# Performance work log

Hardware: AMD Instinct MI355X
Metric: run time of the kernel (lower is better)

Reference implementation:

```python
import jax, jax.numpy as jnp
import numpy as np


def _pairwise_sq(x, y):
    # squared euclidean distances [B,N,M] via gram trick (avoids [B,N,M,D] temp)
    x2 = jnp.sum(x * x, -1)[:, :, None]
    y2 = jnp.sum(y * y, -1)[:, None, :]
    return x2 + y2 - 2.0 * jnp.einsum('bnd,bmd->bnm', x, y)


def _dtw_dp(C):
    # Subsequence DTW accumulated-cost matrix. C: [N,M].
    # D[0,:] = C[0,:] (free start anywhere in y);
    # D[i,j] = C[i,j] + min(D[i-1,j], D[i-1,j-1], D[i,j-1]).
    # Within-row recurrence D[i,j] = min(a[j], D[i,j-1] + C[i,j]) with
    # a[j] = min(D[i-1,j], D[i-1,j-1]) + C[i,j] is a min-plus prefix scan:
    # D[i,j] = S[j] + cummin(a - S)[j], S = cumsum(C[i]).
    inf = jnp.asarray(jnp.inf, C.dtype)
    def row(Dprev, Crow):
        shifted = jnp.concatenate([jnp.full((1,), inf, C.dtype), Dprev[:-1]])
        a = jnp.minimum(Dprev, shifted) + Crow
        S = jnp.cumsum(Crow)
        D = S + jax.lax.cummin(a - S)
        return D, D
    _, Dr = jax.lax.scan(row, C[0], C[1:])
    return jnp.concatenate([C[0][None], Dr], 0)


def _backtrack(D):
    # Backtrack optimal subseq-DTW path from (N-1, argmin D[-1]) to row 0.
    # Returns, per x index i, the largest y index aligned to i on the path
    # (== last occurrence kept by dict(dtw_path) in the torch code).
    N, M = D.shape
    inf = jnp.asarray(jnp.inf, D.dtype)
    j0 = jnp.argmin(D[-1]).astype(jnp.int32)
    i0 = jnp.asarray(N - 1, jnp.int32)
    yl = jnp.zeros((N,), jnp.int32).at[i0].set(j0)
    def step(carry, _):
        i, j, yl = carry
        dd = jnp.where(j > 0, D[i - 1, j - 1], inf)
        du = D[i - 1, j]
        dl = jnp.where(j > 0, D[i, j - 1], inf)
        best = jnp.minimum(jnp.minimum(dd, du), dl)
        take_d = dd == best
        take_u = (~take_d) & (du == best)
        ni = jnp.where(take_d | take_u, i - 1, i)
        nj = jnp.where(take_d, j - 1, jnp.where(take_u, j, j - 1))
        active = i > 0
        ni = jnp.where(active, ni, i)
        nj = jnp.where(active, nj, j)
        yl = jnp.where(active, yl.at[ni].max(nj), yl)
        return (ni, nj, yl), None
    (_, _, yl), _ = jax.lax.scan(step, (i0, j0, yl), None, length=N + M)
    return yl


def setup_inputs() -> dict:
    key = jax.random.key(0)
    k0, k1, k2, k3 = jax.random.split(key, 4)
    B, N, M, D = 16, 1024, 4096, 64
    return {
        'x': jax.random.normal(k0, (B, N, D), jnp.float32),
        'y': jax.random.normal(k1, (B, M, D), jnp.float32),
        'x_t': jax.random.uniform(k2, (B, N), dtype=jnp.float32),
        'y_t': jax.random.uniform(k3, (B, M), dtype=jnp.float32),
    }


def reference(x, y, x_t, y_t):
    C = _pairwise_sq(x, y)                      # [B,N,M]
    D = jax.vmap(_dtw_dp)(C)                    # [B,N,M]
    # total path cost == DP optimum (sum of C along the optimal path)
    dtw_cost = jnp.min(D[:, -1, :], axis=-1)    # [B]
    y_last = jax.vmap(_backtrack)(jax.lax.stop_gradient(D))  # [B,N] int32
    w_ts = x_t                                  # path covers all x indices 0..N-1 in order
    w_vs = jnp.take_along_axis(y_t, y_last, axis=1)
    return dtw_cost, w_ts, w_vs
```

## Files before the change

### kernel.cpp

```cpp
#include <hip/hip_runtime.h>

#define B_ 16
#define N_ 1024
#define M_ 4096
#define D_ 64
#define SROWS_ (N_ + 63)
#define SROWSP_ (SROWS_ + 17)
#define SPAIR_ 544
#define TSB_ ((size_t)SPAIR_ * 128)
#define BTQ_ 96
#define BTROWS_ 128

__device__ __forceinline__ float finf() { return __builtin_inff(); }

__device__ __forceinline__ float wave_shr1(float x) {
  return __int_as_float(__builtin_amdgcn_update_dpp(
      0, __float_as_int(x), 0x138, 0xF, 0xF, false));
}
__device__ __forceinline__ float rdlane(float v, int l) {
  return __int_as_float(__builtin_amdgcn_readlane(__float_as_int(v), l));
}

__global__ void prep_kernel(const float* __restrict__ x,
                            const float* __restrict__ x_t,
                            float* __restrict__ x2,
                            float* __restrict__ w_ts_out) {
  int id = blockIdx.x * blockDim.x + threadIdx.x;
  const float4* xr = (const float4*)(x + (size_t)id * D_);
  float s = 0.f;
#pragma unroll
  for (int e = 0; e < D_ / 4; ++e) {
    float4 v = xr[e];
    s += v.x * v.x + v.y * v.y + v.z * v.z + v.w * v.w;
  }
  x2[id] = s;
  w_ts_out[id] = x_t[id];
}

__global__ __launch_bounds__(256) void gemm_kernel(
    const float* __restrict__ x, const float* __restrict__ y,
    const float* __restrict__ x2, float* __restrict__ Cs, int chunkBase) {
  const int b = blockIdx.z;
  const int tile = blockIdx.x;
  const int t = threadIdx.x;
  const int cg = t & 63;
  const int rg = t >> 6;
  const int ibeg = blockIdx.y * 32;
  float* CsT = Cs + (size_t)(b * 4 + tile) * SROWSP_ * 256;

  __shared__ float4 ylds[16 * 256];
  __shared__ float4 xlds[16 * 32];
  __shared__ float y2lds[256];

  {
    const int j = chunkBase + tile * 256 + t;
    const float4* yrow = (const float4*)(y + ((size_t)b * M_ + j) * D_);
    float4 yr[16];
#pragma unroll
    for (int e = 0; e < 16; ++e) yr[e] = yrow[e];
    float y2 = 0.f;
#pragma unroll
    for (int e = 0; e < 16; ++e)
      y2 += yr[e].x * yr[e].x + yr[e].y * yr[e].y + yr[e].z * yr[e].z +
            yr[e].w * yr[e].w;
    y2lds[t] = y2;
#pragma unroll
    for (int e = 0; e < 16; ++e) ylds[e * 256 + t] = yr[e];
  }
  if (t < 128) {
    const int row = t >> 2;
    const int part = t & 3;
    const float4* xr = (const float4*)(x + ((size_t)b * N_ + ibeg + row) * D_);
#pragma unroll
    for (int k = 0; k < 4; ++k) {
      const int e = part * 4 + k;
      xlds[e * 32 + row] = xr[e];
    }
  }
  __syncthreads();

  const int r0 = rg * 8;
  float acc[8][4];
#pragma unroll
  for (int r = 0; r < 8; ++r)
#pragma unroll
    for (int c = 0; c < 4; ++c) acc[r][c] = 0.f;

#pragma unroll
  for (int kb = 0; kb < 4; ++kb) {
    float4 yf[4][4];
#pragma unroll
    for (int c = 0; c < 4; ++c)
#pragma unroll
      for (int ee = 0; ee < 4; ++ee)
        yf[c][ee] = ylds[(kb * 4 + ee) * 256 + cg + 64 * c];
#pragma unroll
    for (int r = 0; r < 8; ++r) {
      float4 xv[4];
#pragma unroll
      for (int ee = 0; ee < 4; ++ee)
        xv[ee] = xlds[(kb * 4 + ee) * 32 + r0 + r];
#pragma unroll
      for (int ee = 0; ee < 4; ++ee) {
#pragma unroll
        for (int c = 0; c < 4; ++c) {
          acc[r][c] += xv[ee].x * yf[c][ee].x + xv[ee].y * yf[c][ee].y +
                       xv[ee].z * yf[c][ee].z + xv[ee].w * yf[c][ee].w;
        }
      }
    }
  }

#pragma unroll
  for (int r = 0; r < 8; ++r) {
    const int i = ibeg + r0 + r;
    const float xx = x2[b * N_ + i];
#pragma unroll
    for (int c = 0; c < 4; ++c) {
      const int ct = cg + 64 * c;
      const int l = ct >> 2;
      CsT[(size_t)(i + l) * 256 + ct] = xx + y2lds[ct] - 2.f * acc[r][c];
    }
  }
}

__global__ __launch_bounds__(256) void dtw_dp(
    const float* __restrict__ Cs, unsigned char* __restrict__ dec,
    const float* __restrict__ carryIn, float* __restrict__ carryOut,
    float* __restrict__ partV, int* __restrict__ partJ,
    int chunk, int hasCarry) {
  const int b = blockIdx.x;
  const int t = threadIdx.x;
  const int lane = t & 63;
  const int W = t >> 6;

  __shared__ float ring[3][1024];
  __shared__ float cring[1024];
  __shared__ int prog[3];
  __shared__ float redV[4];
  __shared__ int redJ[4];
  volatile int* vProg = prog;

  if (t < 3) prog[t] = -1;
  const float* cIn = carryIn + b * N_;
  if (hasCarry) ((float4*)cring)[t] = ((const float4*)cIn)[t];
  __syncthreads();

  const float INF = finf();
  const float* loadP = Cs + (size_t)(b * 4 + W) * SROWSP_ * 256;
  const int tileG = chunk * 4 + W;
  unsigned short* decP =
      (unsigned short*)(dec + (size_t)(b * 16 + tileG) * TSB_) + lane;
  float* carryB = carryOut + b * N_;
  const int jbase = tileG * 256 + lane * 4;

  float4 cc0 = ((const float4*)(loadP + 0 * 256))[lane];
  float4 cc1 = ((const float4*)(loadP + 1 * 256))[lane];
  float4 cc2 = ((const float4*)(loadP + 2 * 256))[lane];
  float4 cc3 = ((const float4*)(loadP + 3 * 256))[lane];
  float4 cc4 = ((const float4*)(loadP + 4 * 256))[lane];
  float4 cc5 = ((const float4*)(loadP + 5 * 256))[lane];
  float4 cc6 = ((const float4*)(loadP + 6 * 256))[lane];
  float4 cc7 = ((const float4*)(loadP + 7 * 256))[lane];
  loadP += 8 * 256;

  float edgeVec = INF, lvPrev = INF;
  float up0 = 0.f, up1 = 0.f, up2 = 0.f, up3 = 0.f;
  float dpp1 = INF, dpp2 = INF;
  float fin0 = INF, fin1 = INF, fin2 = INF, fin3 = INF;
  float ebuf[8];

#define SUPERHEAD()                                                           \
  {                                                                           \
    if (W > 0) {                                                              \
      if (sb < N_) {                                                          \
        const int tgt = sb + 63;                                              \
        while (vProg[W - 1] < tgt) {}                                         \
        asm volatile("" ::: "memory");                                        \
        edgeVec = ring[W - 1][(sb + lane) & 1023];                            \
      }                                                                       \
    } else if (hasCarry) {                                                    \
      if (sb < N_) edgeVec = cring[(sb + lane) & 1023];                       \
    }                                                                         \
  }

#define DPSTEP(KK, CCV, ROW0, FIN)                                            \
  {                                                                           \
    const float lv = rdlane(edgeVec, u0 + (KK));                              \
    const float left = (lane == 0) ? lv : dpp1;                               \
    const float diag = (lane == 0) ? lvPrev : dpp2;                           \
    lvPrev = lv;                                                              \
    float bv0 = fminf(diag, fminf(up0, left));                                \
    unsigned int pk = (diag <= bv0) ? 0u : ((up0 <= bv0) ? 1u : 2u);          \
    if (ROW0) bv0 = (sb + (KK) == lane) ? 0.f : bv0;                          \
    const float D0 = CCV.x + bv0;                                             \
    float bv1 = fminf(up0, fminf(up1, D0));                                   \
    pk |= (up0 <= bv1) ? 0u : ((up1 <= bv1) ? 4u : 8u);                       \
    if (ROW0) bv1 = (sb + (KK) == lane) ? 0.f : bv1;                          \
    const float D1 = CCV.y + bv1;                                             \
    float bv2 = fminf(up1, fminf(up2, D1));                                   \
    pk |= (up1 <= bv2) ? 0u : ((up2 <= bv2) ? 16u : 32u);                     \
    if (ROW0) bv2 = (sb + (KK) == lane) ? 0.f : bv2;                          \
    const float D2 = CCV.z + bv2;                                             \
    float bv3 = fminf(up2, fminf(up3, D2));                                   \
    pk |= (up2 <= bv3) ? 0u : ((up3 <= bv3) ? 64u : 128u);                    \
    if (ROW0) bv3 = (sb + (KK) == lane) ? 0.f : bv3;                          \
    const float D3 = CCV.w + bv3;                                             \
    ebuf[(KK)] = D3;                                                          \
    if ((KK) & 1) {                                                           \
      pk16 |= pk << 8;                                                        \
      decP[((KK) >> 1) * 64] = (unsigned short)pk16;                          \
    } else {                                                                  \
      pk16 = pk;                                                              \
    }                                                                         \
    if (FIN) {                                                                \
      const bool lr = (sb + (KK) == 1023 + lane);                             \
      fin0 = lr ? D0 : fin0; fin1 = lr ? D1 : fin1;                           \
      fin2 = lr ? D2 : fin2; fin3 = lr ? D3 : fin3;                           \
    }                                                                         \
    const float sh = wave_shr1(D3);                                           \
    dpp2 = dpp1; dpp1 = sh;                                                   \
    up0 = D0; up1 = D1; up2 = D2; up3 = D3;                                   \
    CCV = ((const float4*)(loadP + (KK) * 256))[lane];                        \
  }

#define BLOCKEND()                                                            \
  {                                                                           \
    const int r0 = sb - 63;                                                   \
    if (W < 3) {                                                              \
      if (lane == 63 && r0 > -8 && r0 < N_) {                                 \
        _Pragma("unroll") for (int k = 0; k < 8; ++k) {                       \
          const int r = r0 + k;                                               \
          if ((unsigned)r < (unsigned)N_) ring[W][r] = ebuf[k];               \
        }                                                                     \
        __builtin_amdgcn_s_waitcnt(0xC07F);                                   \
        vProg[W] = r0 + 7;                                                    \
      }                                                                       \
    } else if (chunk < 3) {                                                   \
      if (lane == 63 && r0 > -8 && r0 < N_) {                                 \
        _Pragma("unroll") for (int k = 0; k < 8; ++k) {                       \
          const int r = r0 + k;                                               \
          if ((unsigned)r < (unsigned)N_) carryB[r] = ebuf[k];                \
        }                                                                     \
      }                                                                       \
    }                                                                         \
    loadP += 8 * 256;                                                         \
    decP += 256;                                                              \
  }

#define STEP8(R0, FN)                                                         \
  DPSTEP(0, cc0, R0, FN) DPSTEP(1, cc1, R0, FN) DPSTEP(2, cc2, R0, FN)        \
  DPSTEP(3, cc3, R0, FN) DPSTEP(4, cc4, R0, FN) DPSTEP(5, cc5, R0, FN)        \
  DPSTEP(6, cc6, R0, FN) DPSTEP(7, cc7, R0, FN)

  int sb = 0;
  {
    SUPERHEAD();
    for (int blk = 0; blk < 8; ++blk) {
      const int u0 = blk * 8;
      unsigned int pk16;
      STEP8(1, 0)
      BLOCKEND();
      sb += 8;
    }
  }
  for (int sup = 1; sup < 15; ++sup) {
    SUPERHEAD();
    for (int blk = 0; blk < 8; ++blk) {
      const int u0 = blk * 8;
      unsigned int pk16;
      STEP8(0, 0)
      BLOCKEND();
      sb += 8;
    }
  }
  for (int sup = 15; sup < 17; ++sup) {
    SUPERHEAD();
    for (int blk = 0; blk < 8; ++blk) {
      const int u0 = blk * 8;
      unsigned int pk16;
      STEP8(0, 1)
      BLOCKEND();
      sb += 8;
    }
  }
#undef DPSTEP
#undef STEP8
#undef SUPERHEAD
#undef BLOCKEND

  float mv = fin0; int mj = jbase;
  if (fin1 < mv) { mv = fin1; mj = jbase + 1; }
  if (fin2 < mv) { mv = fin2; mj = jbase + 2; }
  if (fin3 < mv) { mv = fin3; mj = jbase + 3; }
#pragma unroll
  for (int off = 32; off > 0; off >>= 1) {
    const float ov = __shfl_down(mv, off);
    const int oj = __shfl_down(mj, off);
    if (ov < mv || (ov == mv && oj < mj)) { mv = ov; mj = oj; }
  }
  if (lane == 0) { redV[W] = mv; redJ[W] = mj; }
  __syncthreads();
  if (t == 0) {
    float bm = redV[0]; int bj = redJ[0];
#pragma unroll
    for (int w = 1; w < 4; ++w)
      if (redV[w] < bm) { bm = redV[w]; bj = redJ[w]; }
    partV[b * 4 + chunk] = bm;
    partJ[b * 4 + chunk] = bj;
  }
}

__global__ __launch_bounds__(64) void backtrack_kernel(
    const unsigned char* __restrict__ dec, const float* __restrict__ partV,
    const int* __restrict__ partJ, int nch, const float* __restrict__ y_t,
    float* __restrict__ w_vs, float* __restrict__ cost_out) {
  const int b = blockIdx.x;
  const int lane = threadIdx.x;
  __shared__ unsigned int stage[3 * 3072];
  __shared__ unsigned short tab[BTROWS_][BTQ_ * 4 + 2];
  __shared__ int st_i, st_j;
  __shared__ int jrow[BTROWS_ + 1];
  const unsigned char* db = dec + (size_t)b * 16 * TSB_;
  const float* yt = y_t + b * M_;
  float* wv = w_vs + b * N_;

  if (lane == 0) {
    float bc = finf(); int bj = 0;
    for (int c = 0; c < nch; ++c) {
      const float v = partV[b * nch + c];
      const int j = partJ[b * nch + c];
      if (v < bc) { bc = v; bj = j; }
    }
    cost_out[b] = bc;
    st_i = N_ - 1;
    st_j = bj;
    wv[N_ - 1] = yt[bj];
  }
  for (;;) {
    __syncthreads();
    const int i = st_i, j = st_j;
    if (i <= 0) break;
    const int qj = j >> 2;
    int qlo = qj - (BTQ_ - 1);
    if (qlo < 0) qlo = 0;
    const int Tbase = qlo >> 6;
    int plo = (i - 127) >> 1;
    if (plo < 0) plo = 0;

#pragma unroll
    for (int tt = 0; tt < 3; ++tt) {
      int T = Tbase + tt;
      if (T > 15) T = 15;
      const uint4* src =
          (const uint4*)(db + (size_t)T * TSB_ + (size_t)plo * 128);
#pragma unroll
      for (int v = 0; v < 12; ++v) {
        const int wb = tt * 12288 + (v * 64 + lane) * 16;
        const int sw = wb ^ (((wb >> 7) & 7) << 4);
        *(uint4*)((char*)stage + sw) = src[v * 64 + lane];
      }
    }
    __syncthreads();

    const unsigned char* sb8 = (const unsigned char*)stage;
#pragma unroll
    for (int half = 0; half < 2; ++half) {
      const int r = i - lane - half * 64;
      if (r >= 1) {
        unsigned char wr[BTQ_];
#pragma unroll
        for (int k = 0; k < BTQ_; ++k) {
          const int q = qlo + k;
          const int tt = (q >> 6) - Tbase;
          const int l = q & 63;
          const int s = r + l;
          int idx = tt * 12288 + ((s >> 1) - plo) * 128 + l * 2 + (s & 1);
          idx ^= ((idx >> 7) & 7) << 4;
          wr[k] = sb8[idx];
        }
        unsigned short run = 0xFFFF;
        const int tr = lane + half * 64;
#pragma unroll
        for (int k = 0; k < BTQ_; ++k) {
          const unsigned int byte = wr[k];
#pragma unroll
          for (int cs = 0; cs < 4; ++cs) {
            const unsigned int code = (byte >> (2 * cs)) & 3u;
            const int c = 4 * k + cs;
            const unsigned short v =
                (code != 2u) ? (unsigned short)((c << 2) | code) : run;
            tab[tr][c] = v;
            run = v;
          }
        }
      }
    }
    __syncthreads();
    if (lane == 0) {
      const int base = qlo << 2;
      int rr = i, cj = j;
      while (rr >= 1 && (i - rr) < BTROWS_) {
        const int l = i - rr;
        const int c = cj - base;
        if (c < 0) break;
        const unsigned short v = tab[l][c];
        if (v == 0xFFFF) { cj = base - 1; break; }
        const int e = v >> 2;
        const int ce = v & 3;
        cj = base + e - (ce == 0 ? 1 : 0);
        --rr;
        jrow[i - rr] = cj;
      }
      st_i = rr;
      st_j = cj;
    }
    __syncthreads();
    const int cnt = i - st_i;
    if (lane < cnt) wv[i - 1 - lane] = yt[jrow[lane + 1]];
    {
      const int l2 = lane + 64;
      if (l2 < cnt) wv[i - 1 - l2] = yt[jrow[l2 + 1]];
    }
  }
}

extern "C" void kernel_launch(void* const* d_in, const int* in_sizes, int n_in,
                              void* d_out, int out_size, void* d_ws, size_t ws_size,
                              hipStream_t stream) {
  const float* x = (const float*)d_in[0];
  const float* y = (const float*)d_in[1];
  const float* x_t = (const float*)d_in[2];
  const float* y_t = (const float*)d_in[3];

  float* out_cost = (float*)d_out;
  float* out_wts = out_cost + B_;
  float* out_wvs = out_wts + B_ * N_;

  const size_t csBytes = (size_t)B_ * 4 * SROWSP_ * 256 * 4;
  const size_t decBytes = (size_t)B_ * 16 * TSB_;
  const size_t x2Bytes = (size_t)B_ * N_ * 4;

  char* ws = (char*)d_ws;
  float* Cs = (float*)ws;
  unsigned char* dec = (unsigned char*)(ws + csBytes);
  float* x2 = (float*)(ws + csBytes + decBytes);
  float* carryA = (float*)(ws + csBytes + decBytes + x2Bytes);
  float* carryB = carryA + B_ * N_;
  float* partV = carryB + B_ * N_;
  int* partJ = (int*)(partV + B_ * 4);

  prep_kernel<<<dim3((B_ * N_) / 256), 256, 0, stream>>>(x, x_t, x2, out_wts);

  float* cbuf[2] = {carryA, carryB};
  for (int c = 0; c < 4; ++c) {
    gemm_kernel<<<dim3(4, N_ / 32, B_), 256, 0, stream>>>(x, y, x2, Cs,
                                                          c * 1024);
    const float* cin = cbuf[(c + 1) & 1];
    float* cout = cbuf[c & 1];
    dtw_dp<<<dim3(B_), 256, 0, stream>>>(Cs, dec, cin, cout, partV, partJ, c,
                                         c > 0 ? 1 : 0);
  }

  backtrack_kernel<<<dim3(B_), 64, 0, stream>>>(dec, partV, partJ, 4, y_t,
                                                out_wvs, out_cost);
}
```

Baseline: 1.258 ms.

## Pack two batches per DTW block and sync wave pipeline per 8-row block

The DTW wavefront kernel now runs two batch elements per 512-thread workgroup, halving the grid to 8 blocks, with per-group LDS rings and progress flags. Inter-wave synchronization now waits for only 8 new rows of the previous wave's edge values before each 8-row block, instead of 64 rows per super-block. This shortens pipeline fill latency between the four wavefronts. It also co-locates two batches on one CU. That may increase contention or reduce parallelism across CUs, and it adds more frequent spin-waits and edge reloads.

```diff
diff --git a/kernel.cpp b/kernel.cpp
--- a/kernel.cpp
+++ b/kernel.cpp
@@ -4,6 +4,7 @@
 #define N_ 1024
 #define M_ 4096
 #define D_ 64
+#define NB_ 2
 #define SROWS_ (N_ + 63)
 #define SROWSP_ (SROWS_ + 17)
 #define SPAIR_ 544
@@ -124,26 +125,28 @@
   }
 }
 
-__global__ __launch_bounds__(256) void dtw_dp(
+__global__ __launch_bounds__(512) void dtw_dp(
     const float* __restrict__ Cs, unsigned char* __restrict__ dec,
     const float* __restrict__ carryIn, float* __restrict__ carryOut,
     float* __restrict__ partV, int* __restrict__ partJ,
     int chunk, int hasCarry) {
-  const int b = blockIdx.x;
   const int t = threadIdx.x;
-  const int lane = t & 63;
-  const int W = t >> 6;
-
-  __shared__ float ring[3][1024];
-  __shared__ float cring[1024];
-  __shared__ int prog[3];
-  __shared__ float redV[4];
-  __shared__ int redJ[4];
-  volatile int* vProg = prog;
-
-  if (t < 3) prog[t] = -1;
+  const int tb = t & 255;
+  const int G = t >> 8;
+  const int b = blockIdx.x * NB_ + G;
+  const int lane = tb & 63;
+  const int W = tb >> 6;
+
+  __shared__ float ring[NB_][3][1024];
+  __shared__ float cring[NB_][1024];
+  __shared__ int prog[NB_][3];
+  __shared__ float redV[NB_][4];
+  __shared__ int redJ[NB_][4];
+  volatile int* vProg = prog[G];
+
+  if (tb < 3) prog[G][tb] = -1;
   const float* cIn = carryIn + b * N_;
-  if (hasCarry) ((float4*)cring)[t] = ((const float4*)cIn)[t];
+  if (hasCarry) ((float4*)cring[G])[tb] = ((const float4*)cIn)[tb];
   __syncthreads();
 
   const float INF = finf();
@@ -170,23 +173,25 @@
   float fin0 = INF, fin1 = INF, fin2 = INF, fin3 = INF;
   float ebuf[8];
 
-#define SUPERHEAD()                                                           \
+#define BLOCKHEAD()                                                           \
   {                                                                           \
     if (W > 0) {                                                              \
       if (sb < N_) {                                                          \
-        const int tgt = sb + 63;                                              \
+        const int tgt = sb + 7;                                               \
         while (vProg[W - 1] < tgt) {}                                         \
         asm volatile("" ::: "memory");                                        \
-        edgeVec = ring[W - 1][(sb + lane) & 1023];                            \
+        lvPrev = rdlane(edgeVec, 7);                                          \
+        edgeVec = ring[G][W - 1][(sb + lane) & 1023];                         \
       }                                                                       \
     } else if (hasCarry) {                                                    \
-      if (sb < N_) edgeVec = cring[(sb + lane) & 1023];                       \
+      lvPrev = rdlane(edgeVec, 7);                                            \
+      if (sb < N_) edgeVec = cring[G][(sb + lane) & 1023];                    \
     }                                                                         \
   }
 
 #define DPSTEP(KK, CCV, ROW0, FIN)                                            \
   {                                                                           \
-    const float lv = rdlane(edgeVec, u0 + (KK));                              \
+    const float lv = rdlane(edgeVec, (KK));                                   \
     const float left = (lane == 0) ? lv : dpp1;                               \
     const float diag = (lane == 0) ? lvPrev : dpp2;                           \
     lvPrev = lv;                                                              \
@@ -231,7 +236,7 @@
       if (lane == 63 && r0 > -8 && r0 < N_) {                                 \
         _Pragma("unroll") for (int k = 0; k < 8; ++k) {                       \
           const int r = r0 + k;                                               \
-          if ((unsigned)r < (unsigned)N_) ring[W][r] = ebuf[k];               \
+          if ((unsigned)r < (unsigned)N_) ring[G][W][r] = ebuf[k];            \
         }                                                                     \
         __builtin_amdgcn_s_waitcnt(0xC07F);                                   \
         vProg[W] = r0 + 7;                                                    \
@@ -254,39 +259,27 @@
   DPSTEP(6, cc6, R0, FN) DPSTEP(7, cc7, R0, FN)
 
   int sb = 0;
-  {
-    SUPERHEAD();
-    for (int blk = 0; blk < 8; ++blk) {
-      const int u0 = blk * 8;
-      unsigned int pk16;
-      STEP8(1, 0)
-      BLOCKEND();
-      sb += 8;
-    }
-  }
-  for (int sup = 1; sup < 15; ++sup) {
-    SUPERHEAD();
-    for (int blk = 0; blk < 8; ++blk) {
-      const int u0 = blk * 8;
-      unsigned int pk16;
-      STEP8(0, 0)
-      BLOCKEND();
-      sb += 8;
-    }
-  }
-  for (int sup = 15; sup < 17; ++sup) {
-    SUPERHEAD();
-    for (int blk = 0; blk < 8; ++blk) {
-      const int u0 = blk * 8;
-      unsigned int pk16;
-      STEP8(0, 1)
-      BLOCKEND();
-      sb += 8;
-    }
+  for (; sb < 64; sb += 8) {
+    BLOCKHEAD();
+    unsigned int pk16;
+    STEP8(1, 0)
+    BLOCKEND();
+  }
+  for (; sb < 1016; sb += 8) {
+    BLOCKHEAD();
+    unsigned int pk16;
+    STEP8(0, 0)
+    BLOCKEND();
+  }
+  for (; sb < 1088; sb += 8) {
+    BLOCKHEAD();
+    unsigned int pk16;
+    STEP8(0, 1)
+    BLOCKEND();
   }
 #undef DPSTEP
 #undef STEP8
-#undef SUPERHEAD
+#undef BLOCKHEAD
 #undef BLOCKEND
 
   float mv = fin0; int mj = jbase;
@@ -299,13 +292,13 @@
     const int oj = __shfl_down(mj, off);
     if (ov < mv || (ov == mv && oj < mj)) { mv = ov; mj = oj; }
   }
-  if (lane == 0) { redV[W] = mv; redJ[W] = mj; }
+  if (lane == 0) { redV[G][W] = mv; redJ[G][W] = mj; }
   __syncthreads();
-  if (t == 0) {
-    float bm = redV[0]; int bj = redJ[0];
+  if (tb == 0) {
+    float bm = redV[G][0]; int bj = redJ[G][0];
 #pragma unroll
     for (int w = 1; w < 4; ++w)
-      if (redV[w] < bm) { bm = redV[w]; bj = redJ[w]; }
+      if (redV[G][w] < bm) { bm = redV[G][w]; bj = redJ[G][w]; }
     partV[b * 4 + chunk] = bm;
     partJ[b * 4 + chunk] = bj;
   }
@@ -458,8 +451,9 @@
                                                           c * 1024);
     const float* cin = cbuf[(c + 1) & 1];
     float* cout = cbuf[c & 1];
-    dtw_dp<<<dim3(B_), 256, 0, stream>>>(Cs, dec, cin, cout, partV, partJ, c,
-                                         c > 0 ? 1 : 0);
+    dtw_dp<<<dim3(B_ / NB_), 256 * NB_, 0, stream>>>(Cs, dec, cin, cout,
+                                                     partV, partJ, c,
+                                                     c > 0 ? 1 : 0);
   }
 
   backtrack_kernel<<<dim3(B_), 64, 0, stream>>>(dec, partV, partJ, 4, y_t,
```

Result: slower. 1.304 ms (+3.7%).
